# Kernel tuning notes

Hardware: AMD Instinct MI355X
Metric: run time of the kernel (lower is better)

Reference implementation:

```python
import jax, jax.numpy as jnp
import numpy as np

DIM = 16  # scale_size[0] * scale_size[1]
SCALE = DIM ** -0.5


def setup_inputs() -> dict:
    key = jax.random.key(0)
    k1, k2 = jax.random.split(key)
    x = jax.random.normal(k1, (16, 256, 256, 64), dtype=jnp.float32)
    # torch Linear(dim, 2*dim, bias=False): weight shape [32, 16]
    w_qkv = jax.random.normal(k2, (32, 16), dtype=jnp.float32) * (DIM ** -0.5)
    return {"x": x, "w_qkv": w_qkv}


def reference(x, w_qkv):
    B, H, W, C = x.shape
    sh, sw = 4, 4  # scale_size
    # permute to (b, c, h, w) then adaptive avg pool to (4, 4)
    xp = jnp.transpose(x, (0, 3, 1, 2))  # [B, C, H, W]
    pooled = xp.reshape(B, C, sh, H // sh, sw, W // sw).mean(axis=(3, 5))  # [B, C, 4, 4]
    tokens = pooled.reshape(B, C, DIM)  # [B, C, 16]
    # to_qkv: Linear with weight [2*dim, dim] -> x @ W^T, then chunk
    qk = jnp.einsum('bcn,dn->bcd', tokens, w_qkv)  # [B, C, 32]
    q, k = qk[..., :DIM], qk[..., DIM:]  # each [B, C, 16]
    dots = jnp.einsum('bin,bjn->bij', q, k) * SCALE  # [B, C, C]
    attn = jax.nn.softmax(dots, axis=-1)  # [B, C, C]
    out = jnp.einsum('bhwc,btc->bhwt', x, attn)  # [B, H, W, C]
    return jax.nn.gelu(out, approximate=False)
```

## Files before the change

kernel.cpp:

```cpp
#include <hip/hip_runtime.h>
#include <math.h>
#include <cstddef>

#define BB   16
#define HH   256
#define WW   256
#define CC   64
#define NTOK 16
#define NDIM 16

#define PART_FLOATS (BB * NTOK * 16 * CC)

typedef float f32x2 __attribute__((ext_vector_type(2)));
typedef float f32x4 __attribute__((ext_vector_type(4)));

__global__ __launch_bounds__(256) void pool_partial(const float* __restrict__ x,
                                                    float* __restrict__ part) {
    const int blk = blockIdx.x;
    const int rc  = blk & 15;
    const int n   = (blk >> 4) & 15;
    const int b   = blk >> 8;
    const int ph  = n >> 2, pw = n & 3;
    const int t   = threadIdx.x;
    const int c4  = (t & 15) << 2;
    const int sub = t >> 4;

    const int h0 = ph * 64 + rc * 4;
    const int w0 = pw * 64;
    const float* xb = x + (((size_t)b * HH + h0) * WW + w0) * CC;

    float4 s = make_float4(0.f, 0.f, 0.f, 0.f);
#pragma unroll
    for (int k = 0; k < 16; ++k) {
        const int pos = sub + (k << 4);
        const int row = pos >> 6;
        const int col = pos & 63;
        const float4 v = *(const float4*)(xb + ((size_t)row * WW + col) * CC + c4);
        s.x += v.x; s.y += v.y; s.z += v.z; s.w += v.w;
    }

    __shared__ float lds[16 * 64];
    lds[sub * 64 + c4 + 0] = s.x;
    lds[sub * 64 + c4 + 1] = s.y;
    lds[sub * 64 + c4 + 2] = s.z;
    lds[sub * 64 + c4 + 3] = s.w;
    __syncthreads();

    if (t < 64) {
        float acc = 0.f;
#pragma unroll
        for (int ss = 0; ss < 16; ++ss) acc += lds[ss * 64 + t];
        part[(((size_t)b * NTOK + n) * 16 + rc) * CC + t] = acc;
    }
}

__global__ __launch_bounds__(256) void attn_kernel(const float* __restrict__ part,
                                                   const float* __restrict__ w_qkv,
                                                   float* __restrict__ attnT) {
    const int b = blockIdx.x;
    const int t = threadIdx.x;

    __shared__ float tok[CC * NDIM];
    __shared__ float ql [CC * NDIM];
    __shared__ float kl [CC * NDIM];
    __shared__ float dl [CC * CC];
    __shared__ float rs [CC];

    const float* pb = part + (size_t)b * NTOK * 16 * CC;

    for (int idx = t; idx < CC * NDIM; idx += 256) {
        const int c = idx >> 4, n = idx & 15;
        float a = 0.f;
#pragma unroll
        for (int rc = 0; rc < 16; ++rc) a += pb[((size_t)n * 16 + rc) * CC + c];
        tok[c * NDIM + n] = a * (1.0f / 4096.0f);
    }
    __syncthreads();

    for (int idx = t; idx < CC * 32; idx += 256) {
        const int c = idx >> 5, d = idx & 31;
        float a = 0.f;
#pragma unroll
        for (int n = 0; n < NDIM; ++n) a += tok[c * NDIM + n] * w_qkv[d * NDIM + n];
        if (d < 16) ql[c * NDIM + d] = a;
        else        kl[c * NDIM + (d - 16)] = a;
    }
    __syncthreads();

    for (int idx = t; idx < CC * CC; idx += 256) {
        const int i = idx >> 6, j = idx & 63;
        float a = 0.f;
#pragma unroll
        for (int n = 0; n < NDIM; ++n) a += ql[i * NDIM + n] * kl[j * NDIM + n];
        dl[idx] = a * 0.25f;
    }
    __syncthreads();

    if (t < CC) {
        float m = -1e30f;
        for (int j = 0; j < CC; ++j) m = fmaxf(m, dl[t * CC + j]);
        float ssum = 0.f;
        for (int j = 0; j < CC; ++j) {
            const float e = expf(dl[t * CC + j] - m);
            dl[t * CC + j] = e;
            ssum += e;
        }
        rs[t] = 1.0f / ssum;
    }
    __syncthreads();

    for (int idx = t; idx < CC * CC; idx += 256) {
        const int tt = idx & 63;
        attnT[(size_t)b * (CC * CC) + idx] = dl[tt * CC + (idx >> 6)] * rs[tt];
    }
}

__device__ __forceinline__ float gelu_exact(float v) {
    return 0.5f * v * (1.0f + erff(v * 0.70710678118654752f));
}

#define XPAD 65

__global__ __launch_bounds__(256) void out_kernel(const float* __restrict__ x,
                                                  const float* __restrict__ attnT,
                                                  float* __restrict__ out) {
    const int tid  = threadIdx.x;
    const int lane = tid & 63;
    const int th   = __builtin_amdgcn_readfirstlane(tid >> 6);
    const int blk  = blockIdx.x;
    const int b    = blk >> 10;
    const size_t pixbase = (size_t)blk * 64;

    __shared__ float xt[64 * XPAD];

    const float4* xsrc = (const float4*)(x + pixbase * CC);
#pragma unroll
    for (int it = 0; it < 4; ++it) {
        const int i  = tid + it * 256;
        const float4 v = xsrc[i];
        const int px = i >> 4;
        const int c0 = (i << 2) & 63;
        float* d = &xt[px * XPAD + c0];
        d[0] = v.x; d[1] = v.y; d[2] = v.z; d[3] = v.w;
    }
    __syncthreads();

    const float* __restrict__ at = attnT + (size_t)b * (CC * CC) + th * 16;
    const float* __restrict__ xr = &xt[lane * XPAD];

    f32x2 a0 = {0.f, 0.f};
    f32x2 a1 = a0, a2 = a0, a3 = a0, a4 = a0, a5 = a0, a6 = a0, a7 = a0;

#pragma unroll 4
    for (int c = 0; c < CC; ++c) {
        const float xc = xr[c];
        f32x2 xc2; xc2.x = xc; xc2.y = xc;
        const f32x2* w = (const f32x2*)(at + c * CC);
        asm("v_pk_fma_f32 %0, %1, %2, %0" : "+v"(a0) : "s"(w[0]), "v"(xc2));
        asm("v_pk_fma_f32 %0, %1, %2, %0" : "+v"(a1) : "s"(w[1]), "v"(xc2));
        asm("v_pk_fma_f32 %0, %1, %2, %0" : "+v"(a2) : "s"(w[2]), "v"(xc2));
        asm("v_pk_fma_f32 %0, %1, %2, %0" : "+v"(a3) : "s"(w[3]), "v"(xc2));
        asm("v_pk_fma_f32 %0, %1, %2, %0" : "+v"(a4) : "s"(w[4]), "v"(xc2));
        asm("v_pk_fma_f32 %0, %1, %2, %0" : "+v"(a5) : "s"(w[5]), "v"(xc2));
        asm("v_pk_fma_f32 %0, %1, %2, %0" : "+v"(a6) : "s"(w[6]), "v"(xc2));
        asm("v_pk_fma_f32 %0, %1, %2, %0" : "+v"(a7) : "s"(w[7]), "v"(xc2));
    }

    float* op = out + (pixbase + lane) * CC + th * 16;
    float4 g;
    g.x = gelu_exact(a0.x); g.y = gelu_exact(a0.y); g.z = gelu_exact(a1.x); g.w = gelu_exact(a1.y);
    ((float4*)op)[0] = g;
    g.x = gelu_exact(a2.x); g.y = gelu_exact(a2.y); g.z = gelu_exact(a3.x); g.w = gelu_exact(a3.y);
    ((float4*)op)[1] = g;
    g.x = gelu_exact(a4.x); g.y = gelu_exact(a4.y); g.z = gelu_exact(a5.x); g.w = gelu_exact(a5.y);
    ((float4*)op)[2] = g;
    g.x = gelu_exact(a6.x); g.y = gelu_exact(a6.y); g.z = gelu_exact(a7.x); g.w = gelu_exact(a7.y);
    ((float4*)op)[3] = g;
}

extern "C" void kernel_launch(void* const* d_in, const int* in_sizes, int n_in,
                              void* d_out, int out_size, void* d_ws, size_t ws_size,
                              hipStream_t stream) {
    const float* x     = (const float*)d_in[0];
    const float* w_qkv = (const float*)d_in[1];
    float* out   = (float*)d_out;
    float* part  = (float*)d_ws;
    float* attnT = part + PART_FLOATS;

    pool_partial<<<BB * NTOK * 16, 256, 0, stream>>>(x, part);
    attn_kernel<<<BB, 256, 0, stream>>>(part, w_qkv, attnT);
    out_kernel<<<BB * 256 * 4, 256, 0, stream>>>(x, attnT, out);
}
```

Before: 553.6 us.

## Use split-bf16 MFMA for the output mixing matmul with pre-packed attention fragments

The per-pixel 64x64 channel mix moves from scalar-broadcast packed FP32 FMAs to bf16 MFMA 16x16x32 instructions. Both operands are split into hi and lo bf16 parts and three cross products are accumulated, to keep close to fp32 accuracy. The attention kernel now writes the attention matrix pre-split and pre-swizzled into MFMA B-fragment layout, so the output kernel only copies it into LDS. The output kernel also loads x directly into registers with prefetch instead of staging it through padded LDS. This trades extra conversion ALU work and some precision for tensor-core throughput, in a kernel that is likely memory-bound anyway.

```diff
diff --git a/kernel.cpp b/kernel.cpp
--- a/kernel.cpp
+++ b/kernel.cpp
@@ -10,9 +10,18 @@
 #define NDIM 16
 
 #define PART_FLOATS (BB * NTOK * 16 * CC)
-
-typedef float f32x2 __attribute__((ext_vector_type(2)));
+#define FRAG_USHORT_PER_B (16 * 64 * 8)
+
+typedef short s16x8 __attribute__((ext_vector_type(8)));
 typedef float f32x4 __attribute__((ext_vector_type(4)));
+
+__device__ __forceinline__ unsigned short f2bf_rne(float f) {
+    unsigned int u = __float_as_uint(f);
+    return (unsigned short)((u + 0x7fffu + ((u >> 16) & 1u)) >> 16);
+}
+__device__ __forceinline__ float bf2f(unsigned short h) {
+    return __uint_as_float(((unsigned int)h) << 16);
+}
 
 __global__ __launch_bounds__(256) void pool_partial(const float* __restrict__ x,
                                                     float* __restrict__ part) {
@@ -56,7 +65,7 @@
 
 __global__ __launch_bounds__(256) void attn_kernel(const float* __restrict__ part,
                                                    const float* __restrict__ w_qkv,
-                                                   float* __restrict__ attnT) {
+                                                   unsigned short* __restrict__ fragw) {
     const int b = blockIdx.x;
     const int t = threadIdx.x;
 
@@ -109,9 +118,25 @@
     }
     __syncthreads();
 
-    for (int idx = t; idx < CC * CC; idx += 256) {
-        const int tt = idx & 63;
-        attnT[(size_t)b * (CC * CC) + idx] = dl[tt * CC + (idx >> 6)] * rs[tt];
+    for (int idx = t; idx < 512; idx += 256) {
+        const int tt   = idx >> 3;
+        const int oct  = idx & 7;
+        const int ks   = oct >> 2;
+        const int g    = oct & 3;
+        const int slot = ((tt >> 4) * 2 + ks) * 2;
+        const int lanei = (tt & 15) + g * 16;
+        const float rr = rs[tt];
+        s16x8 hi, lo;
+#pragma unroll
+        for (int j = 0; j < 8; ++j) {
+            const float w = dl[tt * CC + oct * 8 + j] * rr;
+            const unsigned short h = f2bf_rne(w);
+            hi[j] = (short)h;
+            lo[j] = (short)f2bf_rne(w - bf2f(h));
+        }
+        s16x8* dst = (s16x8*)fragw + ((size_t)b * 16 + slot) * 64;
+        dst[lanei]      = hi;
+        dst[64 + lanei] = lo;
     }
 }
 
@@ -119,63 +144,77 @@
     return 0.5f * v * (1.0f + erff(v * 0.70710678118654752f));
 }
 
-#define XPAD 65
-
-__global__ __launch_bounds__(256) void out_kernel(const float* __restrict__ x,
-                                                  const float* __restrict__ attnT,
-                                                  float* __restrict__ out) {
+__device__ __forceinline__ void split8(const float4 v0, const float4 v1,
+                                       s16x8& hi, s16x8& lo) {
+    const float f[8] = {v0.x, v0.y, v0.z, v0.w, v1.x, v1.y, v1.z, v1.w};
+#pragma unroll
+    for (int j = 0; j < 8; ++j) {
+        const unsigned short h = f2bf_rne(f[j]);
+        hi[j] = (short)h;
+        lo[j] = (short)f2bf_rne(f[j] - bf2f(h));
+    }
+}
+
+__global__ __launch_bounds__(256) void out_mfma(const float* __restrict__ x,
+                                                const unsigned short* __restrict__ frag,
+                                                float* __restrict__ out) {
     const int tid  = threadIdx.x;
     const int lane = tid & 63;
-    const int th   = __builtin_amdgcn_readfirstlane(tid >> 6);
+    const int wv   = tid >> 6;
     const int blk  = blockIdx.x;
-    const int b    = blk >> 10;
-    const size_t pixbase = (size_t)blk * 64;
-
-    __shared__ float xt[64 * XPAD];
-
-    const float4* xsrc = (const float4*)(x + pixbase * CC);
-#pragma unroll
-    for (int it = 0; it < 4; ++it) {
-        const int i  = tid + it * 256;
-        const float4 v = xsrc[i];
-        const int px = i >> 4;
-        const int c0 = (i << 2) & 63;
-        float* d = &xt[px * XPAD + c0];
-        d[0] = v.x; d[1] = v.y; d[2] = v.z; d[3] = v.w;
-    }
-    __syncthreads();
-
-    const float* __restrict__ at = attnT + (size_t)b * (CC * CC) + th * 16;
-    const float* __restrict__ xr = &xt[lane * XPAD];
-
-    f32x2 a0 = {0.f, 0.f};
-    f32x2 a1 = a0, a2 = a0, a3 = a0, a4 = a0, a5 = a0, a6 = a0, a7 = a0;
-
-#pragma unroll 4
-    for (int c = 0; c < CC; ++c) {
-        const float xc = xr[c];
-        f32x2 xc2; xc2.x = xc; xc2.y = xc;
-        const f32x2* w = (const f32x2*)(at + c * CC);
-        asm("v_pk_fma_f32 %0, %1, %2, %0" : "+v"(a0) : "s"(w[0]), "v"(xc2));
-        asm("v_pk_fma_f32 %0, %1, %2, %0" : "+v"(a1) : "s"(w[1]), "v"(xc2));
-        asm("v_pk_fma_f32 %0, %1, %2, %0" : "+v"(a2) : "s"(w[2]), "v"(xc2));
-        asm("v_pk_fma_f32 %0, %1, %2, %0" : "+v"(a3) : "s"(w[3]), "v"(xc2));
-        asm("v_pk_fma_f32 %0, %1, %2, %0" : "+v"(a4) : "s"(w[4]), "v"(xc2));
-        asm("v_pk_fma_f32 %0, %1, %2, %0" : "+v"(a5) : "s"(w[5]), "v"(xc2));
-        asm("v_pk_fma_f32 %0, %1, %2, %0" : "+v"(a6) : "s"(w[6]), "v"(xc2));
-        asm("v_pk_fma_f32 %0, %1, %2, %0" : "+v"(a7) : "s"(w[7]), "v"(xc2));
-    }
-
-    float* op = out + (pixbase + lane) * CC + th * 16;
-    float4 g;
-    g.x = gelu_exact(a0.x); g.y = gelu_exact(a0.y); g.z = gelu_exact(a1.x); g.w = gelu_exact(a1.y);
-    ((float4*)op)[0] = g;
-    g.x = gelu_exact(a2.x); g.y = gelu_exact(a2.y); g.z = gelu_exact(a3.x); g.w = gelu_exact(a3.y);
-    ((float4*)op)[1] = g;
-    g.x = gelu_exact(a4.x); g.y = gelu_exact(a4.y); g.z = gelu_exact(a5.x); g.w = gelu_exact(a5.y);
-    ((float4*)op)[2] = g;
-    g.x = gelu_exact(a6.x); g.y = gelu_exact(a6.y); g.z = gelu_exact(a7.x); g.w = gelu_exact(a7.y);
-    ((float4*)op)[3] = g;
+    const int b    = blk >> 8;
+    const int row  = lane & 15;
+    const int g    = lane >> 4;
+
+    __shared__ unsigned short bfr[16 * 64 * 8];
+    {
+        const s16x8* s = (const s16x8*)(frag + (size_t)b * FRAG_USHORT_PER_B);
+        s16x8* d = (s16x8*)bfr;
+#pragma unroll
+        for (int it = 0; it < 4; ++it) d[tid + it * 256] = s[tid + it * 256];
+    }
+    __syncthreads();
+
+    const size_t pix0 = (size_t)blk * 256 + wv * 64;
+    const float* xb = x + (pix0 + row) * CC + g * 8;
+    float* ob = out + (pix0 + (g << 2)) * CC + row;
+
+    float4 c0 = *(const float4*)(xb);
+    float4 c1 = *(const float4*)(xb + 4);
+    float4 c2 = *(const float4*)(xb + 32);
+    float4 c3 = *(const float4*)(xb + 36);
+
+    for (int rb = 0; rb < 4; ++rb) {
+        s16x8 ah0, al0, ah1, al1;
+        split8(c0, c1, ah0, al0);
+        split8(c2, c3, ah1, al1);
+        if (rb < 3) {
+            const float* nx = xb + (size_t)(rb + 1) * 16 * CC;
+            c0 = *(const float4*)(nx);
+            c1 = *(const float4*)(nx + 4);
+            c2 = *(const float4*)(nx + 32);
+            c3 = *(const float4*)(nx + 36);
+        }
+#pragma unroll
+        for (int tcol = 0; tcol < 4; ++tcol) {
+            const s16x8 bh0 = *(const s16x8*)&bfr[((((tcol * 2 + 0) * 2 + 0) * 64) + lane) * 8];
+            const s16x8 bl0 = *(const s16x8*)&bfr[((((tcol * 2 + 0) * 2 + 1) * 64) + lane) * 8];
+            const s16x8 bh1 = *(const s16x8*)&bfr[((((tcol * 2 + 1) * 2 + 0) * 64) + lane) * 8];
+            const s16x8 bl1 = *(const s16x8*)&bfr[((((tcol * 2 + 1) * 2 + 1) * 64) + lane) * 8];
+            f32x4 acc = {0.f, 0.f, 0.f, 0.f};
+            acc = __builtin_amdgcn_mfma_f32_16x16x32_bf16(ah0, bh0, acc, 0, 0, 0);
+            acc = __builtin_amdgcn_mfma_f32_16x16x32_bf16(ah1, bh1, acc, 0, 0, 0);
+            acc = __builtin_amdgcn_mfma_f32_16x16x32_bf16(al0, bh0, acc, 0, 0, 0);
+            acc = __builtin_amdgcn_mfma_f32_16x16x32_bf16(al1, bh1, acc, 0, 0, 0);
+            acc = __builtin_amdgcn_mfma_f32_16x16x32_bf16(ah0, bl0, acc, 0, 0, 0);
+            acc = __builtin_amdgcn_mfma_f32_16x16x32_bf16(ah1, bl1, acc, 0, 0, 0);
+
+            float* o = ob + (size_t)rb * 16 * CC + tcol * 16;
+#pragma unroll
+            for (int r = 0; r < 4; ++r)
+                o[(size_t)r * CC] = gelu_exact(acc[r]);
+        }
+    }
 }
 
 extern "C" void kernel_launch(void* const* d_in, const int* in_sizes, int n_in,
@@ -185,9 +224,9 @@
     const float* w_qkv = (const float*)d_in[1];
     float* out   = (float*)d_out;
     float* part  = (float*)d_ws;
-    float* attnT = part + PART_FLOATS;
+    unsigned short* frag = (unsigned short*)(part + PART_FLOATS);
 
     pool_partial<<<BB * NTOK * 16, 256, 0, stream>>>(x, part);
-    attn_kernel<<<BB, 256, 0, stream>>>(part, w_qkv, attnT);
-    out_kernel<<<BB * 256 * 4, 256, 0, stream>>>(x, attnT, out);
-}
+    attn_kernel<<<BB, 256, 0, stream>>>(part, w_qkv, frag);
+    out_mfma<<<BB * 256, 256, 0, stream>>>(x, frag, out);
+}
```

Result: faster. 507.3 us (-8.4%).
